# Kernel optimization log

Measured on AMD Instinct MI355X. Metric: run time of the kernel, lower is better.

Reference implementation:

```python
import jax, jax.numpy as jnp
import numpy as np

N = 100000
E = 1600000


def _sage_conv(x, src, tgt, W_l, b, W_r):
    # PyG SAGEConv (mean aggr): out = lin_l(mean_{j in N(i)} x_j) + lin_r(x_i)
    msg = x[src]                                            # [E, F] gather
    agg = jax.ops.segment_sum(msg, tgt, num_segments=N)     # [N, F]
    deg = jax.ops.segment_sum(jnp.ones((src.shape[0],), x.dtype), tgt, num_segments=N)
    agg = agg / jnp.maximum(deg, 1.0)[:, None]               # mean
    return agg @ W_l + b + x @ W_r


def setup_inputs() -> dict:
    key = jax.random.key(0)
    ks = jax.random.split(key, 16)
    d = {
        "x": jax.random.normal(ks[0], (N, 9), jnp.float32),
        "edge_index": jax.random.randint(ks[1], (2, E), 0, N, jnp.int32).astype(jnp.int64),
        "W1_l": jax.random.normal(ks[2], (9, 128), jnp.float32) / np.sqrt(9),
        "b1": jnp.zeros((128,), jnp.float32),
        "W1_r": jax.random.normal(ks[3], (9, 128), jnp.float32) / np.sqrt(9),
        "W2_l": jax.random.normal(ks[4], (128, 128), jnp.float32) / np.sqrt(128),
        "b2": jnp.zeros((128,), jnp.float32),
        "W2_r": jax.random.normal(ks[5], (128, 128), jnp.float32) / np.sqrt(128),
        "W3_l": jax.random.normal(ks[6], (128, 128), jnp.float32) / np.sqrt(128),
        "b3": jnp.zeros((128,), jnp.float32),
        "W3_r": jax.random.normal(ks[7], (128, 128), jnp.float32) / np.sqrt(128),
        "Wl1": jax.random.normal(ks[8], (128, 128), jnp.float32) / np.sqrt(128),
        "bl1": jnp.zeros((128,), jnp.float32),
        "Wl2": jax.random.normal(ks[9], (128, 64), jnp.float32) / np.sqrt(128),
        "bl2": jnp.zeros((64,), jnp.float32),
        "Wl3": jax.random.normal(ks[10], (64, 3), jnp.float32) / np.sqrt(64),
        "bl3": jnp.zeros((3,), jnp.float32),
    }
    return d


def reference(x, edge_index, W1_l, b1, W1_r, W2_l, b2, W2_r, W3_l, b3, W3_r,
              Wl1, bl1, Wl2, bl2, Wl3, bl3):
    src, tgt = edge_index[0], edge_index[1]
    h = jax.nn.relu(_sage_conv(x, src, tgt, W1_l, b1, W1_r))   # dropout = identity (eval)
    h = jax.nn.relu(_sage_conv(h, src, tgt, W2_l, b2, W2_r))
    h = jax.nn.relu(_sage_conv(h, src, tgt, W3_l, b3, W3_r))
    h = jax.nn.relu(h @ Wl1 + bl1)
    h = jax.nn.relu(h @ Wl2 + bl2)
    h = h @ Wl3 + bl3
    return jax.nn.log_softmax(h, axis=-1)
```

## Files before the change

### kernel.cpp

```cpp
#include <hip/hip_runtime.h>
#include <hip/hip_fp16.h>
#include <stdint.h>

typedef _Float16 f16x8 __attribute__((ext_vector_type(8)));
typedef float f32x4 __attribute__((ext_vector_type(4)));


#define CH 16384
#define MAXNB 1024

__global__ __launch_bounds__(256) void bhist_k(const int* __restrict__ ei,
        int* __restrict__ bh, int E, int shift, int NB, int NBLK) {
    __shared__ int lh[MAXNB];
    for (int b = threadIdx.x; b < NB; b += 256) lh[b] = 0;
    __syncthreads();
    int base = blockIdx.x * CH;
    int end = min(base + CH, E);
    for (int e = base + threadIdx.x; e < end; e += 256) {
        int t = ei[(size_t)E + e];
        atomicAdd(&lh[t >> shift], 1);
    }
    __syncthreads();
    for (int b = threadIdx.x; b < NB; b += 256)
        bh[(size_t)b * NBLK + blockIdx.x] = lh[b];
}

__global__ void scan_col_k(int* bh, int* __restrict__ btot, int NBLK, int NB) {
    __shared__ int sd[128];
    int b = blockIdx.x;
    int t = threadIdx.x;
    int v = (t < NBLK) ? bh[(size_t)b * NBLK + t] : 0;
    sd[t] = v;
    __syncthreads();
    for (int off = 1; off < 128; off <<= 1) {
        int x = (t >= off) ? sd[t - off] : 0;
        __syncthreads();
        sd[t] += x;
        __syncthreads();
    }
    if (t < NBLK) bh[(size_t)b * NBLK + t] = sd[t] - v;
    if (t == 127) btot[b] = sd[127];
}

__global__ void scan_block_k(const int* __restrict__ deg, int* __restrict__ excl,
                             int* __restrict__ bsum, int N) {
    __shared__ int sd[256];
    int t = threadIdx.x;
    int base = blockIdx.x * 1024 + t * 4;
    int v0 = (base + 0 < N) ? deg[base + 0] : 0;
    int v1 = (base + 1 < N) ? deg[base + 1] : 0;
    int v2 = (base + 2 < N) ? deg[base + 2] : 0;
    int v3 = (base + 3 < N) ? deg[base + 3] : 0;
    int s = v0 + v1 + v2 + v3;
    sd[t] = s;
    __syncthreads();
    for (int off = 1; off < 256; off <<= 1) {
        int x = (t >= off) ? sd[t - off] : 0;
        __syncthreads();
        sd[t] += x;
        __syncthreads();
    }
    int incl = sd[t];
    int ex = incl - s;
    if (base + 0 < N) excl[base + 0] = ex;
    if (base + 1 < N) excl[base + 1] = ex + v0;
    if (base + 2 < N) excl[base + 2] = ex + v0 + v1;
    if (base + 3 < N) excl[base + 3] = ex + v0 + v1 + v2;
    if (t == 255) bsum[blockIdx.x] = incl;
}

__global__ __launch_bounds__(256) void bscatter_k(const int* __restrict__ ei,
        const int* __restrict__ bh, const int* __restrict__ bbase,
        int* __restrict__ staged, int E, int shift, int NB, int NBLK) {
    __shared__ int cur[MAXNB];
    for (int b = threadIdx.x; b < NB; b += 256)
        cur[b] = bbase[b] + bh[(size_t)b * NBLK + blockIdx.x];
    __syncthreads();
    int base = blockIdx.x * CH;
    int end = min(base + CH, E);
    int mask = (1 << shift) - 1;
    for (int e = base + threadIdx.x; e < end; e += 256) {
        int s = ei[e];
        int t = ei[(size_t)E + e];
        int p = atomicAdd(&cur[t >> shift], 1);
        staged[p] = s | ((t & mask) << 17);
    }
}

__global__ __launch_bounds__(256) void csrfill_k(const int* __restrict__ staged,
        const int* __restrict__ bbase, int* __restrict__ rs, int* __restrict__ csr,
        int N, int E, int shift, int NB) {
    __shared__ int lh[256];
    __shared__ int sd[256];
    int b = blockIdx.x;
    int tpb = 1 << shift;
    int t0 = b << shift;
    int s0 = bbase[b];
    int s1 = (b == NB - 1) ? E : bbase[b + 1];
    int t = threadIdx.x;
    if (t < tpb) lh[t] = 0;
    __syncthreads();
    for (int e = s0 + t; e < s1; e += 256)
        atomicAdd(&lh[staged[e] >> 17], 1);
    __syncthreads();
    int v = (t < tpb) ? lh[t] : 0;
    sd[t] = v;
    __syncthreads();
    for (int off = 1; off < 256; off <<= 1) {
        int x = (t >= off) ? sd[t - off] : 0;
        __syncthreads();
        sd[t] += x;
        __syncthreads();
    }
    if (t < tpb) {
        int excl = sd[t] - v;
        lh[t] = excl;
        int tg = t0 + t;
        if (tg < N) rs[tg] = s0 + excl;
    }
    if (b == NB - 1 && t == 0) rs[N] = E;
    __syncthreads();
    for (int e = s0 + t; e < s1; e += 256) {
        int w = staged[e];
        int lt = w >> 17;
        int src = w & 0x1FFFF;
        int p = s0 + atomicAdd(&lh[lt], 1);
        csr[p] = src;
    }
}


__global__ void agg9pack_k(const float* __restrict__ x, const int* __restrict__ rs,
                           const int* __restrict__ csr, __half* __restrict__ a32,
                           int N) {
    int i = blockIdx.x * blockDim.x + threadIdx.x;
    if (i >= N) return;
    int s0 = rs[i], s1 = rs[i + 1];
    float a[9];
    #pragma unroll
    for (int f = 0; f < 9; ++f) a[f] = 0.f;
    for (int j = s0; j < s1; ++j) {
        const float* p = x + (size_t)csr[j] * 9;
        #pragma unroll
        for (int f = 0; f < 9; ++f) a[f] += p[f];
    }
    float inv = (s1 > s0) ? 1.f / (float)(s1 - s0) : 0.f;
    const float* xr = x + (size_t)i * 9;
    union { _Float16 h[32]; uint4 u4[4]; } o;
    #pragma unroll
    for (int f = 0; f < 9; ++f) o.h[f] = (_Float16)(a[f] * inv);
    #pragma unroll
    for (int f = 0; f < 9; ++f) o.h[9 + f] = (_Float16)xr[f];
    #pragma unroll
    for (int f = 18; f < 32; ++f) o.h[f] = (_Float16)0.f;
    uint4* dst = reinterpret_cast<uint4*>(a32 + (size_t)i * 32);
    #pragma unroll
    for (int q = 0; q < 4; ++q) dst[q] = o.u4[q];
}

__global__ __launch_bounds__(256) void agg128h4_k(const __half* __restrict__ h16,
        const int* __restrict__ rs, const int* __restrict__ csr,
        __half* __restrict__ out, int N) {
    int l16 = threadIdx.x & 15;
    int node = blockIdx.x * 16 + (threadIdx.x >> 4);
    if (node >= N) return;
    int s0 = rs[node], s1 = rs[node + 1];
    const uint4* h4 = reinterpret_cast<const uint4*>(h16);
    float acc[8];
    #pragma unroll
    for (int c = 0; c < 8; ++c) acc[c] = 0.f;
    int j = s0;
    for (; j + 8 <= s1; j += 8) {
        int n[8];
        #pragma unroll
        for (int u = 0; u < 8; ++u) n[u] = csr[j + u];
        uint4 v[8];
        #pragma unroll
        for (int u = 0; u < 8; ++u)
            v[u] = h4[(size_t)n[u] * 16 + l16];
        #pragma unroll
        for (int u = 0; u < 8; ++u) {
            const __half2* p = reinterpret_cast<const __half2*>(&v[u]);
            #pragma unroll
            for (int q = 0; q < 4; ++q) {
                float2 f = __half22float2(p[q]);
                acc[q * 2]     += f.x;
                acc[q * 2 + 1] += f.y;
            }
        }
    }
    for (; j + 4 <= s1; j += 4) {
        uint4 v[4];
        #pragma unroll
        for (int u = 0; u < 4; ++u)
            v[u] = h4[(size_t)csr[j + u] * 16 + l16];
        #pragma unroll
        for (int u = 0; u < 4; ++u) {
            const __half2* p = reinterpret_cast<const __half2*>(&v[u]);
            #pragma unroll
            for (int q = 0; q < 4; ++q) {
                float2 f = __half22float2(p[q]);
                acc[q * 2]     += f.x;
                acc[q * 2 + 1] += f.y;
            }
        }
    }
    for (; j < s1; ++j) {
        uint4 vv = h4[(size_t)csr[j] * 16 + l16];
        const __half2* p = reinterpret_cast<const __half2*>(&vv);
        #pragma unroll
        for (int q = 0; q < 4; ++q) {
            float2 f = __half22float2(p[q]);
            acc[q * 2]     += f.x;
            acc[q * 2 + 1] += f.y;
        }
    }
    float inv = (s1 > s0) ? 1.f / (float)(s1 - s0) : 0.f;
    __half2 o[4];
    #pragma unroll
    for (int q = 0; q < 4; ++q)
        o[q] = __floats2half2_rn(acc[q * 2] * inv, acc[q * 2 + 1] * inv);
    reinterpret_cast<uint4*>(out)[(size_t)node * 16 + l16] =
        *reinterpret_cast<uint4*>(o);
}


struct WPD { const float* W; _Float16* dst; int K, N; };
struct WPD6 { WPD d[6]; };

__global__ void wpack6_k(WPD6 all) {
    WPD w = all.d[blockIdx.y];
    int idx = blockIdx.x * blockDim.x + threadIdx.x;
    int kcb = w.K / 32;
    int total = (w.N / 16) * kcb * 64;
    if (idx >= total) return;
    int lane = idx & 63;
    int blk = idx >> 6;
    int kb = blk % kcb;
    int nf = blk / kcb;
    int col = nf * 16 + (lane & 15);
    int k0 = kb * 32 + (lane >> 4) * 8;
    f16x8 v;
    #pragma unroll
    for (int j = 0; j < 8; ++j)
        v[j] = (_Float16)w.W[(size_t)(k0 + j) * w.N + col];
    *reinterpret_cast<f16x8*>(w.dst + (size_t)idx * 8) = v;
}

__global__ void wpack1_k(const float* __restrict__ Wl, const float* __restrict__ Wr,
                         _Float16* __restrict__ wpk) {
    int idx = blockIdx.x * blockDim.x + threadIdx.x;
    if (idx >= 8 * 64) return;
    int lane = idx & 63;
    int nf = idx >> 6;
    int col = nf * 16 + (lane & 15);
    int k0 = (lane >> 4) * 8;
    f16x8 v;
    #pragma unroll
    for (int j = 0; j < 8; ++j) {
        int k = k0 + j;
        float w = (k < 9) ? Wl[(size_t)k * 128 + col]
                : (k < 18) ? Wr[(size_t)(k - 9) * 128 + col] : 0.f;
        v[j] = (_Float16)w;
    }
    *reinterpret_cast<f16x8*>(wpk + (size_t)idx * 8) = v;
}

template<int NF, int NS, int KK>
__global__ __launch_bounds__(256) void mfma_lin_k(
        const __half* A1, const __half* A2,
        const _Float16* __restrict__ pk1, const _Float16* __restrict__ pk2,
        const float* __restrict__ bias, __half* C, int M) {
    constexpr int TN = 64 * NF;
    constexpr int KB = KK / 32;
    constexpr int LPR = KK / 8;
    constexpr int RPI = 256 / LPR;
    constexpr int ITER = 64 / RPI;
    __shared__ _Float16 a_lds[NS][64][KK + 8];

    int tid = threadIdx.x;
    int lane = tid & 63;
    int wave = tid >> 6;
    int rb = blockIdx.x * 64;

    const __half* As[2] = {A1, A2};
    #pragma unroll
    for (int s = 0; s < NS; ++s) {
        #pragma unroll
        for (int i = 0; i < ITER; ++i) {
            int row = (tid / LPR) + i * RPI;
            int c = tid % LPR;
            int grow = rb + row;
            uint4 v = make_uint4(0, 0, 0, 0);
            if (grow < M)
                v = reinterpret_cast<const uint4*>(As[s] + (size_t)grow * KK)[c];
            *reinterpret_cast<uint4*>(&a_lds[s][row][c * 8]) = v;
        }
    }

    const _Float16* pks[2] = {pk1, pk2};
    f16x8 bfrag[NS][KB][NF];
    #pragma unroll
    for (int s = 0; s < NS; ++s)
        #pragma unroll
        for (int kb = 0; kb < KB; ++kb)
            #pragma unroll
            for (int n = 0; n < NF; ++n) {
                int nf = wave * NF + n;
                bfrag[s][kb][n] =
                    reinterpret_cast<const f16x8*>(pks[s])[(size_t)(nf * KB + kb) * 64 + lane];
            }

    f32x4 acc[4][NF];
    #pragma unroll
    for (int m = 0; m < 4; ++m)
        #pragma unroll
        for (int n = 0; n < NF; ++n)
            acc[m][n] = (f32x4){0.f, 0.f, 0.f, 0.f};

    __syncthreads();

    #pragma unroll
    for (int s = 0; s < NS; ++s)
        #pragma unroll
        for (int kb = 0; kb < KB; ++kb)
            #pragma unroll
            for (int m = 0; m < 4; ++m) {
                f16x8 a = *reinterpret_cast<const f16x8*>(
                    &a_lds[s][m * 16 + (lane & 15)][kb * 32 + (lane >> 4) * 8]);
                #pragma unroll
                for (int n = 0; n < NF; ++n)
                    acc[m][n] = __builtin_amdgcn_mfma_f32_16x16x32_f16(
                        a, bfrag[s][kb][n], acc[m][n], 0, 0, 0);
            }

    #pragma unroll
    for (int n = 0; n < NF; ++n) {
        int col = wave * NF * 16 + n * 16 + (lane & 15);
        float bv = bias[col];
        #pragma unroll
        for (int m = 0; m < 4; ++m) {
            #pragma unroll
            for (int j = 0; j < 4; ++j) {
                int grow = rb + m * 16 + (lane >> 4) * 4 + j;
                if (grow < M) {
                    float v = fmaxf(acc[m][n][j] + bv, 0.f);
                    C[(size_t)grow * TN + col] = __float2half_rn(v);
                }
            }
        }
    }
}

__global__ void final_k(const __half* __restrict__ m2, const float* __restrict__ W,
                        const float* __restrict__ b, float* __restrict__ out, int N) {
    int i = blockIdx.x * blockDim.x + threadIdx.x;
    if (i >= N) return;
    const f16x8* r8 = reinterpret_cast<const f16x8*>(m2 + (size_t)i * 64);
    float l0 = b[0], l1 = b[1], l2 = b[2];
    #pragma unroll
    for (int q = 0; q < 8; ++q) {
        f16x8 v8 = r8[q];
        #pragma unroll
        for (int j = 0; j < 8; ++j) {
            float v = (float)v8[j];
            int k = q * 8 + j;
            l0 = fmaf(v, W[k * 3 + 0], l0);
            l1 = fmaf(v, W[k * 3 + 1], l1);
            l2 = fmaf(v, W[k * 3 + 2], l2);
        }
    }
    float mx = fmaxf(l0, fmaxf(l1, l2));
    float e0 = expf(l0 - mx), e1 = expf(l1 - mx), e2 = expf(l2 - mx);
    float lse = logf(e0 + e1 + e2) + mx;
    out[(size_t)i * 3 + 0] = l0 - lse;
    out[(size_t)i * 3 + 1] = l1 - lse;
    out[(size_t)i * 3 + 2] = l2 - lse;
}


extern "C" void kernel_launch(void* const* d_in, const int* in_sizes, int n_in,
                              void* d_out, int out_size, void* d_ws, size_t ws_size,
                              hipStream_t stream) {
    const float* x   = (const float*)d_in[0];
    const int* ei    = (const int*)d_in[1];
    const float* W1l = (const float*)d_in[2];
    const float* b1  = (const float*)d_in[3];
    const float* W1r = (const float*)d_in[4];
    const float* W2l = (const float*)d_in[5];
    const float* b2  = (const float*)d_in[6];
    const float* W2r = (const float*)d_in[7];
    const float* W3l = (const float*)d_in[8];
    const float* b3  = (const float*)d_in[9];
    const float* W3r = (const float*)d_in[10];
    const float* Wl1 = (const float*)d_in[11];
    const float* bl1 = (const float*)d_in[12];
    const float* Wl2 = (const float*)d_in[13];
    const float* bl2 = (const float*)d_in[14];
    const float* Wl3 = (const float*)d_in[15];
    const float* bl3 = (const float*)d_in[16];
    float* out = (float*)d_out;

    const int N = in_sizes[0] / 9;
    const int E = in_sizes[1] / 2;

    char* ws = (char*)d_ws;
    size_t off = 0;
    auto alloc = [&](size_t bytes) -> void* {
        void* p = ws + off;
        off += (bytes + 255) & ~(size_t)255;
        return p;
    };
    __half* h16    = (__half*)alloc((size_t)N * 128 * sizeof(__half));
    __half* agg16  = (__half*)alloc((size_t)N * 128 * sizeof(__half));
    __half* m16    = (__half*)alloc((size_t)N * 64 * sizeof(__half));
    __half* a32    = (__half*)alloc((size_t)N * 32 * sizeof(__half));
    int* rs     = (int*)alloc((size_t)(N + 1) * sizeof(int));
    int* csr    = (int*)alloc((size_t)E * sizeof(int));
    int* staged = (int*)alloc((size_t)E * sizeof(int));
    _Float16* wpk1  = (_Float16*)alloc(32 * 128 * sizeof(_Float16));
    _Float16* wpk2l = (_Float16*)alloc(128 * 128 * sizeof(_Float16));
    _Float16* wpk2r = (_Float16*)alloc(128 * 128 * sizeof(_Float16));
    _Float16* wpk3l = (_Float16*)alloc(128 * 128 * sizeof(_Float16));
    _Float16* wpk3r = (_Float16*)alloc(128 * 128 * sizeof(_Float16));
    _Float16* wpkl1 = (_Float16*)alloc(128 * 128 * sizeof(_Float16));
    _Float16* wpkl2 = (_Float16*)alloc(128 * 64 * sizeof(_Float16));
    (void)ws_size; (void)n_in; (void)out_size;

    int shift = 7;
    while ((((size_t)N + ((size_t)1 << shift) - 1) >> shift) > MAXNB) ++shift;
    const int NB = (N + (1 << shift) - 1) >> shift;
    const int NBLK = (E + CH - 1) / CH;
    int* bh    = (int*)alloc((size_t)NB * NBLK * sizeof(int));
    int* btot  = (int*)alloc((size_t)NB * sizeof(int));
    int* bbase = (int*)alloc((size_t)(NB + 1) * sizeof(int));
    int* bsum  = (int*)alloc(64 * sizeof(int));

    WPD6 wp;
    wp.d[0] = {W2l, wpk2l, 128, 128};
    wp.d[1] = {W2r, wpk2r, 128, 128};
    wp.d[2] = {W3l, wpk3l, 128, 128};
    wp.d[3] = {W3r, wpk3r, 128, 128};
    wp.d[4] = {Wl1, wpkl1, 128, 128};
    wp.d[5] = {Wl2, wpkl2, 128, 64};
    wpack6_k<<<dim3(8, 6), 256, 0, stream>>>(wp);
    wpack1_k<<<2, 256, 0, stream>>>(W1l, W1r, wpk1);

    bhist_k<<<NBLK, 256, 0, stream>>>(ei, bh, E, shift, NB, NBLK);
    scan_col_k<<<NB, 128, 0, stream>>>(bh, btot, NBLK, NB);
    scan_block_k<<<1, 256, 0, stream>>>(btot, bbase, bsum, NB);
    bscatter_k<<<NBLK, 256, 0, stream>>>(ei, bh, bbase, staged, E, shift, NB, NBLK);
    csrfill_k<<<NB, 256, 0, stream>>>(staged, bbase, rs, csr, N, E, shift, NB);

    const int gemm_grid = (N + 63) / 64;
    const int agg_grid = (N + 15) / 16;

    agg9pack_k<<<(N + 255) / 256, 256, 0, stream>>>(x, rs, csr, a32, N);
    mfma_lin_k<2, 1, 32><<<gemm_grid, 256, 0, stream>>>(
        a32, nullptr, wpk1, nullptr, b1, h16, N);

    agg128h4_k<<<agg_grid, 256, 0, stream>>>(h16, rs, csr, agg16, N);
    mfma_lin_k<2, 2, 128><<<gemm_grid, 256, 0, stream>>>(
        agg16, h16, wpk2l, wpk2r, b2, h16, N);

    agg128h4_k<<<agg_grid, 256, 0, stream>>>(h16, rs, csr, agg16, N);
    mfma_lin_k<2, 2, 128><<<gemm_grid, 256, 0, stream>>>(
        agg16, h16, wpk3l, wpk3r, b3, h16, N);

    mfma_lin_k<2, 1, 128><<<gemm_grid, 256, 0, stream>>>(
        h16, nullptr, wpkl1, nullptr, bl1, h16, N);
    mfma_lin_k<1, 1, 128><<<gemm_grid, 256, 0, stream>>>(
        h16, nullptr, wpkl2, nullptr, bl2, m16, N);
    final_k<<<(N + 255) / 256, 256, 0, stream>>>(m16, Wl3, bl3, out, N);
}
```

Baseline: 312.3 us.

## Fuse final linear into log-softmax, shrink CSR chunk size, drop 8-wide agg unroll

Fuses the 128->64 MFMA linear layer with the 64->3 projection and log-softmax into one kernel, keeping the intermediate in LDS instead of writing and rereading an fp16 buffer. Reduces the CSR-build chunk size from 16384 to 2048 edges, which gives more histogram/scatter blocks, and widens the column scan to 256 threads with 4 values each so it covers up to 1024 blocks. Removes the 8-edge unrolled gather loop in the 128-wide aggregation, leaving the 4-edge loop. The fused tail does its 64x3 dot product with only one wave per block, and the larger histogram table adds scan traffic.

```diff
diff --git a/kernel.cpp b/kernel.cpp
--- a/kernel.cpp
+++ b/kernel.cpp
@@ -6,8 +6,9 @@
 typedef float f32x4 __attribute__((ext_vector_type(4)));
 
 
-#define CH 16384
+#define CH 2048
 #define MAXNB 1024
+#define MAXNBLK 1024
 
 __global__ __launch_bounds__(256) void bhist_k(const int* __restrict__ ei,
         int* __restrict__ bh, int E, int shift, int NB, int NBLK) {
@@ -25,21 +26,31 @@
         bh[(size_t)b * NBLK + blockIdx.x] = lh[b];
 }
 
-__global__ void scan_col_k(int* bh, int* __restrict__ btot, int NBLK, int NB) {
-    __shared__ int sd[128];
-    int b = blockIdx.x;
+__global__ __launch_bounds__(256) void scan_col_k(int* bh, int* __restrict__ btot,
+                                                  int NBLK, int NB) {
+    __shared__ int sd[256];
+    size_t rowoff = (size_t)blockIdx.x * NBLK;
     int t = threadIdx.x;
-    int v = (t < NBLK) ? bh[(size_t)b * NBLK + t] : 0;
-    sd[t] = v;
-    __syncthreads();
-    for (int off = 1; off < 128; off <<= 1) {
+    int base = t * 4;
+    int v0 = (base + 0 < NBLK) ? bh[rowoff + base + 0] : 0;
+    int v1 = (base + 1 < NBLK) ? bh[rowoff + base + 1] : 0;
+    int v2 = (base + 2 < NBLK) ? bh[rowoff + base + 2] : 0;
+    int v3 = (base + 3 < NBLK) ? bh[rowoff + base + 3] : 0;
+    int s = v0 + v1 + v2 + v3;
+    sd[t] = s;
+    __syncthreads();
+    for (int off = 1; off < 256; off <<= 1) {
         int x = (t >= off) ? sd[t - off] : 0;
         __syncthreads();
         sd[t] += x;
         __syncthreads();
     }
-    if (t < NBLK) bh[(size_t)b * NBLK + t] = sd[t] - v;
-    if (t == 127) btot[b] = sd[127];
+    int ex = sd[t] - s;
+    if (base + 0 < NBLK) bh[rowoff + base + 0] = ex;
+    if (base + 1 < NBLK) bh[rowoff + base + 1] = ex + v0;
+    if (base + 2 < NBLK) bh[rowoff + base + 2] = ex + v0 + v1;
+    if (base + 3 < NBLK) bh[rowoff + base + 3] = ex + v0 + v1 + v2;
+    if (t == 255) btot[blockIdx.x] = sd[255];
 }
 
 __global__ void scan_block_k(const int* __restrict__ deg, int* __restrict__ excl,
@@ -170,25 +181,6 @@
     #pragma unroll
     for (int c = 0; c < 8; ++c) acc[c] = 0.f;
     int j = s0;
-    for (; j + 8 <= s1; j += 8) {
-        int n[8];
-        #pragma unroll
-        for (int u = 0; u < 8; ++u) n[u] = csr[j + u];
-        uint4 v[8];
-        #pragma unroll
-        for (int u = 0; u < 8; ++u)
-            v[u] = h4[(size_t)n[u] * 16 + l16];
-        #pragma unroll
-        for (int u = 0; u < 8; ++u) {
-            const __half2* p = reinterpret_cast<const __half2*>(&v[u]);
-            #pragma unroll
-            for (int q = 0; q < 4; ++q) {
-                float2 f = __half22float2(p[q]);
-                acc[q * 2]     += f.x;
-                acc[q * 2 + 1] += f.y;
-            }
-        }
-    }
     for (; j + 4 <= s1; j += 4) {
         uint4 v[4];
         #pragma unroll
@@ -352,30 +344,80 @@
     }
 }
 
-__global__ void final_k(const __half* __restrict__ m2, const float* __restrict__ W,
-                        const float* __restrict__ b, float* __restrict__ out, int N) {
-    int i = blockIdx.x * blockDim.x + threadIdx.x;
-    if (i >= N) return;
-    const f16x8* r8 = reinterpret_cast<const f16x8*>(m2 + (size_t)i * 64);
-    float l0 = b[0], l1 = b[1], l2 = b[2];
-    #pragma unroll
-    for (int q = 0; q < 8; ++q) {
-        f16x8 v8 = r8[q];
-        #pragma unroll
-        for (int j = 0; j < 8; ++j) {
-            float v = (float)v8[j];
-            int k = q * 8 + j;
-            l0 = fmaf(v, W[k * 3 + 0], l0);
-            l1 = fmaf(v, W[k * 3 + 1], l1);
-            l2 = fmaf(v, W[k * 3 + 2], l2);
-        }
-    }
-    float mx = fmaxf(l0, fmaxf(l1, l2));
-    float e0 = expf(l0 - mx), e1 = expf(l1 - mx), e2 = expf(l2 - mx);
-    float lse = logf(e0 + e1 + e2) + mx;
-    out[(size_t)i * 3 + 0] = l0 - lse;
-    out[(size_t)i * 3 + 1] = l1 - lse;
-    out[(size_t)i * 3 + 2] = l2 - lse;
+__global__ __launch_bounds__(256) void mfma_lin_final_k(
+        const __half* A1, const _Float16* __restrict__ pk1,
+        const float* __restrict__ bias,
+        const float* __restrict__ W3, const float* __restrict__ b3,
+        float* __restrict__ outp, int M) {
+    constexpr int KK = 128;
+    __shared__ _Float16 a_lds[64][136];
+    __shared__ float smem[64][68];
+
+    int tid = threadIdx.x;
+    int lane = tid & 63;
+    int wave = tid >> 6;
+    int rb = blockIdx.x * 64;
+
+    #pragma unroll
+    for (int i = 0; i < 4; ++i) {
+        int row = (tid >> 4) + i * 16;
+        int grow = rb + row;
+        uint4 v = make_uint4(0, 0, 0, 0);
+        if (grow < M)
+            v = reinterpret_cast<const uint4*>(A1 + (size_t)grow * KK)[tid & 15];
+        *reinterpret_cast<uint4*>(&a_lds[row][(tid & 15) * 8]) = v;
+    }
+
+    f16x8 bfrag[4];
+    #pragma unroll
+    for (int kb = 0; kb < 4; ++kb)
+        bfrag[kb] = reinterpret_cast<const f16x8*>(pk1)[(size_t)(wave * 4 + kb) * 64 + lane];
+
+    f32x4 acc[4];
+    #pragma unroll
+    for (int m = 0; m < 4; ++m) acc[m] = (f32x4){0.f, 0.f, 0.f, 0.f};
+
+    __syncthreads();
+
+    #pragma unroll
+    for (int kb = 0; kb < 4; ++kb)
+        #pragma unroll
+        for (int m = 0; m < 4; ++m) {
+            f16x8 a = *reinterpret_cast<const f16x8*>(
+                &a_lds[m * 16 + (lane & 15)][kb * 32 + (lane >> 4) * 8]);
+            acc[m] = __builtin_amdgcn_mfma_f32_16x16x32_f16(a, bfrag[kb], acc[m], 0, 0, 0);
+        }
+
+    int col = wave * 16 + (lane & 15);
+    float bv = bias[col];
+    #pragma unroll
+    for (int m = 0; m < 4; ++m)
+        #pragma unroll
+        for (int j = 0; j < 4; ++j) {
+            int row = m * 16 + (lane >> 4) * 4 + j;
+            smem[row][col] = fmaxf(acc[m][j] + bv, 0.f);
+        }
+    __syncthreads();
+
+    if (tid < 64) {
+        int grow = rb + tid;
+        if (grow < M) {
+            float l0 = b3[0], l1 = b3[1], l2 = b3[2];
+            #pragma unroll 8
+            for (int k = 0; k < 64; ++k) {
+                float v = smem[tid][k];
+                l0 = fmaf(v, W3[k * 3 + 0], l0);
+                l1 = fmaf(v, W3[k * 3 + 1], l1);
+                l2 = fmaf(v, W3[k * 3 + 2], l2);
+            }
+            float mx = fmaxf(l0, fmaxf(l1, l2));
+            float e0 = expf(l0 - mx), e1 = expf(l1 - mx), e2 = expf(l2 - mx);
+            float lse = logf(e0 + e1 + e2) + mx;
+            outp[(size_t)grow * 3 + 0] = l0 - lse;
+            outp[(size_t)grow * 3 + 1] = l1 - lse;
+            outp[(size_t)grow * 3 + 2] = l2 - lse;
+        }
+    }
 }
 
 
@@ -413,7 +455,6 @@
     };
     __half* h16    = (__half*)alloc((size_t)N * 128 * sizeof(__half));
     __half* agg16  = (__half*)alloc((size_t)N * 128 * sizeof(__half));
-    __half* m16    = (__half*)alloc((size_t)N * 64 * sizeof(__half));
     __half* a32    = (__half*)alloc((size_t)N * 32 * sizeof(__half));
     int* rs     = (int*)alloc((size_t)(N + 1) * sizeof(int));
     int* csr    = (int*)alloc((size_t)E * sizeof(int));
@@ -447,7 +488,7 @@
     wpack1_k<<<2, 256, 0, stream>>>(W1l, W1r, wpk1);
 
     bhist_k<<<NBLK, 256, 0, stream>>>(ei, bh, E, shift, NB, NBLK);
-    scan_col_k<<<NB, 128, 0, stream>>>(bh, btot, NBLK, NB);
+    scan_col_k<<<NB, 256, 0, stream>>>(bh, btot, NBLK, NB);
     scan_block_k<<<1, 256, 0, stream>>>(btot, bbase, bsum, NB);
     bscatter_k<<<NBLK, 256, 0, stream>>>(ei, bh, bbase, staged, E, shift, NB, NBLK);
     csrfill_k<<<NB, 256, 0, stream>>>(staged, bbase, rs, csr, N, E, shift, NB);
@@ -469,7 +510,6 @@
 
     mfma_lin_k<2, 1, 128><<<gemm_grid, 256, 0, stream>>>(
         h16, nullptr, wpkl1, nullptr, bl1, h16, N);
-    mfma_lin_k<1, 1, 128><<<gemm_grid, 256, 0, stream>>>(
-        h16, nullptr, wpkl2, nullptr, bl2, m16, N);
-    final_k<<<(N + 255) / 256, 256, 0, stream>>>(m16, Wl3, bl3, out, N);
-}
+    mfma_lin_final_k<<<gemm_grid, 256, 0, stream>>>(
+        h16, wpkl2, bl2, Wl3, bl3, out, N);
+}
```

Result: faster. 294.8 us (-5.6%).
